# Optimization experiments

Measured on AMD Instinct MI355X. Metric: run time of the kernel, lower is better.

## Reference

```python
import jax, jax.numpy as jnp
import numpy as np

B, T, C, H = 256, 256, 384, 64
MAX_REL = 3  # max_relative_position hardcoded in module


def setup_inputs() -> dict:
    key = jax.random.key(0)
    ks = jax.random.split(key, 6)
    s = 1.0 / np.sqrt(C)
    return {
        "x": jax.random.normal(ks[0], (B, T, C), dtype=jnp.float32),
        "Wq": jax.random.normal(ks[1], (C, H), dtype=jnp.float32) * s,
        "Wk": jax.random.normal(ks[2], (C, H), dtype=jnp.float32) * s,
        "Wv": jax.random.normal(ks[3], (C, H), dtype=jnp.float32) * s,
        "rel_k_table": jax.random.normal(ks[4], (2 * MAX_REL + 1, H), dtype=jnp.float32) * s,
        "rel_v_table": jax.random.normal(ks[5], (2 * MAX_REL + 1, H), dtype=jnp.float32) * s,
    }


def reference(x, Wq, Wk, Wv, rel_k_table, rel_v_table):
    Bd, Td, Cd = x.shape
    Hd = Wq.shape[1]
    q = x @ Wq  # [B,T,H]
    k = x @ Wk
    v = x @ Wv
    # relative position indices, clipped Shaw-style
    r = jnp.arange(Td)
    idx = jnp.clip(r[None, :] - r[:, None], -MAX_REL, MAX_REL) + MAX_REL  # [T,T]
    rk = rel_k_table[idx]  # [T,T,H]
    rv = rel_v_table[idx]  # [T,T,H]
    attn1 = jnp.einsum('bth,bsh->bts', q, k)
    attn2 = jnp.einsum('bth,tsh->bts', q, rk)
    scale = jnp.sqrt(jnp.asarray(Hd, dtype=x.dtype))
    scores = (attn1 + attn2) / scale
    causal = jnp.tril(jnp.ones((Td, Td), dtype=bool))
    scores = jnp.where(causal[None, :, :], scores, -jnp.inf)
    attn = jax.nn.softmax(scores, axis=-1)  # dropout = identity (eval mode)
    w1 = jnp.einsum('bts,bsh->bth', attn, v)
    w2 = jnp.einsum('bts,tsh->bth', attn, rv)
    return w1 + w2  # [B,T,H]
```

## Files before the change

### kernel.cpp

```cpp
#include <hip/hip_runtime.h>
#include <hip/hip_bf16.h>


typedef __attribute__((ext_vector_type(8))) __bf16 bf16x8;
typedef __attribute__((ext_vector_type(8))) short short8;
typedef __attribute__((ext_vector_type(4))) float f32x4;
typedef __attribute__((ext_vector_type(4))) int   i32x4;

#define MFMA16(A, B, C) __builtin_amdgcn_mfma_f32_16x16x32_bf16((A), (B), (C), 0, 0, 0)

__device__ __forceinline__ unsigned short f2bf(float f) {
    unsigned int u = __builtin_bit_cast(unsigned int, f);
    u = (u + 0x7FFFu + ((u >> 16) & 1u)) >> 16;
    return (unsigned short)u;
}
__device__ __forceinline__ float bf2f(unsigned short s) {
    unsigned int u = ((unsigned int)s) << 16;
    return __builtin_bit_cast(float, u);
}
__device__ __forceinline__ bf16x8 ld16(const unsigned short* p) {
    return __builtin_bit_cast(bf16x8, *(const i32x4*)p);
}

__global__ void prep_wt(const float* __restrict__ Wq, const float* __restrict__ Wk,
                        const float* __restrict__ Wv, const float* __restrict__ relk,
                        unsigned short* __restrict__ Wt, unsigned short* __restrict__ Rk) {
    int i = blockIdx.x * 256 + threadIdx.x;
    if (i < 3 * 64 * 384) {
        int kk = i % 384;
        int h  = (i / 384) & 63;
        int w  = i / (384 * 64);
        const float* W = (w == 0) ? Wq : ((w == 1) ? Wk : Wv);
        Wt[i] = f2bf(W[kk * 64 + h]);
    } else if (i < 3 * 64 * 384 + 1024) {
        int j = i - 3 * 64 * 384;
        int n = j >> 6, h = j & 63;
        Rk[j] = (n < 4) ? f2bf(relk[n * 64 + h]) : (unsigned short)0;
    }
}

__global__ __launch_bounds__(512, 1) void qkv_kernel(
        const float* __restrict__ x, const unsigned short* __restrict__ Wt,
        unsigned short* __restrict__ q, unsigned short* __restrict__ k,
        unsigned short* __restrict__ vT) {
    extern __shared__ unsigned short ws[];

    const int tid  = threadIdx.x;
    const int wave = tid >> 6;
    const int lane = tid & 63;
    const int c    = lane & 15;
    const int quad = lane >> 4;
    const int row0 = blockIdx.x * 128;
    const int myrow = row0 + wave * 16 + c;

    const float* xp0 = x + (size_t)myrow * 384;

    f32x4 xb[2][8];
#pragma unroll
    for (int j = 0; j < 4; j++) {
        xb[0][2 * j]     = *(const f32x4*)(xp0 + j * 32 + quad * 8);
        xb[0][2 * j + 1] = *(const f32x4*)(xp0 + j * 32 + quad * 8 + 4);
    }

#pragma unroll
    for (int it = 0; it < 18; it++) {
        int P = it * 512 + tid;
        int r = P / 48, pc = P % 48;
        i32x4 d = *(const i32x4*)(Wt + r * 384 + pc * 8);
        *(i32x4*)(ws + r * 392 + pc * 8) = d;
    }
    __syncthreads();

    f32x4 zero = {0.f, 0.f, 0.f, 0.f};
    f32x4 aq[4], ak[4], av[4];
#pragma unroll
    for (int i = 0; i < 4; i++) { aq[i] = zero; ak[i] = zero; av[i] = zero; }

#pragma unroll
    for (int ck = 0; ck < 3; ck++) {
        const int cur = ck & 1;
        if (ck < 2) {
#pragma unroll
            for (int j = 0; j < 4; j++) {
                const float* xp = xp0 + (ck + 1) * 128 + j * 32 + quad * 8;
                xb[1 - cur][2 * j]     = *(const f32x4*)xp;
                xb[1 - cur][2 * j + 1] = *(const f32x4*)(xp + 4);
            }
        }
#pragma unroll
        for (int j = 0; j < 4; j++) {
            short8 xs8;
#pragma unroll
            for (int e = 0; e < 4; e++) {
                xs8[e]     = (short)f2bf(xb[cur][2 * j][e]);
                xs8[4 + e] = (short)f2bf(xb[cur][2 * j + 1][e]);
            }
            bf16x8 a = __builtin_bit_cast(bf16x8, xs8);
            const int col = (ck * 4 + j) * 32 + quad * 8;

#pragma unroll
            for (int nt = 0; nt < 4; nt++) {
                bf16x8 bq = ld16(ws + (nt * 16 + c) * 392 + col);
                bf16x8 bk = ld16(ws + (64 + nt * 16 + c) * 392 + col);
                bf16x8 aw = ld16(ws + (128 + nt * 16 + c) * 392 + col);
                aq[nt] = MFMA16(a, bq, aq[nt]);
                ak[nt] = MFMA16(a, bk, ak[nt]);
                av[nt] = MFMA16(aw, a, av[nt]);
            }
        }
    }

    const int b   = row0 >> 8;
    const int t0b = row0 & 255;
#pragma unroll
    for (int nt = 0; nt < 4; nt++) {
#pragma unroll
        for (int r = 0; r < 4; r++) {
            int row = row0 + wave * 16 + quad * 4 + r;
            q[row * 64 + nt * 16 + c] = f2bf(aq[nt][r]);
            k[row * 64 + nt * 16 + c] = f2bf(ak[nt][r]);
            int h = nt * 16 + quad * 4 + r;
            vT[(b * 64 + h) * 256 + t0b + wave * 16 + c] = f2bf(av[nt][r]);
        }
    }
}

__global__ __launch_bounds__(64, 4) void attn_kernel(
        const unsigned short* __restrict__ q, const unsigned short* __restrict__ k,
        const unsigned short* __restrict__ vT, const unsigned short* __restrict__ Rk,
        const float* __restrict__ relv, float* __restrict__ out) {
    __shared__ unsigned short P[16][264];
    __shared__ float E[16][4];

    const int lane = threadIdx.x;
    const int c    = lane & 15;
    const int quad = lane >> 4;
    const int tt   = blockIdx.x;
    const int b    = blockIdx.y;
    const int t0   = tt * 16;
    const int nst  = tt + 1;

    f32x4 zero = {0.f, 0.f, 0.f, 0.f};

    float rv[4][4];
#pragma unroll
    for (int j = 0; j < 4; j++)
#pragma unroll
        for (int nt = 0; nt < 4; nt++) rv[j][nt] = relv[j * 64 + nt * 16 + c];

    const unsigned short* qp = q + (size_t)(b * 256 + t0 + c) * 64 + quad * 8;
    bf16x8 aq0 = ld16(qp);
    bf16x8 aq1 = ld16(qp + 32);

    {
        f32x4 e = zero;
        e = MFMA16(aq0, ld16(Rk + c * 64 + quad * 8), e);
        e = MFMA16(aq1, ld16(Rk + c * 64 + 32 + quad * 8), e);
        if (c < 4) {
#pragma unroll
            for (int r = 0; r < 4; r++) E[quad * 4 + r][c] = e[r];
        }
    }
    __syncthreads();
    f32x4 ef[4];
#pragma unroll
    for (int r = 0; r < 4; r++) ef[r] = *(const f32x4*)(&E[quad * 4 + r][0]);

    float l[4] = {0.f, 0.f, 0.f, 0.f};
#pragma unroll
    for (int st = 0; st < 16; st++) {
        if (st < nst) {
            const unsigned short* kp = k + (size_t)(b * 256 + st * 16 + c) * 64 + quad * 8;
            f32x4 s = zero;
            s = MFMA16(aq0, ld16(kp), s);
            s = MFMA16(aq1, ld16(kp + 32), s);
#pragma unroll
            for (int r = 0; r < 4; r++) {
                int tg = t0 + quad * 4 + r;
                int sg = st * 16 + c;
                int d  = sg - tg;
                float e = (d <= -3) ? ef[r][0] : (d == -2) ? ef[r][1]
                        : (d == -1) ? ef[r][2] : ef[r][3];
                float p = (d > 0) ? 0.f : __expf(0.125f * (s[r] + e));
                l[r] += p;
                P[quad * 4 + r][sg] = f2bf(p);
            }
        }
    }
    if (nst & 1) {
#pragma unroll
        for (int r = 0; r < 4; r++) P[quad * 4 + r][nst * 16 + c] = 0;
    }
#pragma unroll
    for (int r = 0; r < 4; r++)
#pragma unroll
        for (int ofs = 1; ofs < 16; ofs <<= 1)
            l[r] += __shfl_xor(l[r], ofs, 64);
    float rl[4];
#pragma unroll
    for (int r = 0; r < 4; r++) rl[r] = 1.0f / l[r];
    __syncthreads();

    f32x4 o[4];
#pragma unroll
    for (int nt = 0; nt < 4; nt++) o[nt] = zero;
    const int ksteps = (nst + 1) >> 1;
#pragma unroll
    for (int ks = 0; ks < 8; ks++) {
        if (ks < ksteps) {
            bf16x8 ap = ld16(&P[c][ks * 32 + quad * 8]);
#pragma unroll
            for (int nt = 0; nt < 4; nt++) {
                const unsigned short* vp = vT + (size_t)(b * 64 + nt * 16 + c) * 256
                                              + ks * 32 + quad * 8;
                o[nt] = MFMA16(ap, ld16(vp), o[nt]);
            }
        }
    }

#pragma unroll
    for (int r = 0; r < 4; r++) {
        int tl = quad * 4 + r;
        int tg = t0 + tl;
        float pa = (tg >= 2) ? bf2f(P[tl][tg - 2]) * rl[r] : 0.f;
        float pb = (tg >= 1) ? bf2f(P[tl][tg - 1]) * rl[r] : 0.f;
        float pc = bf2f(P[tl][tg]) * rl[r];
#pragma unroll
        for (int nt = 0; nt < 4; nt++) {
            float r0 = rv[0][nt];
            float w2 = r0 + pa * (rv[1][nt] - r0) + pb * (rv[2][nt] - r0)
                          + pc * (rv[3][nt] - r0);
            out[(size_t)(b * 256 + tg) * 64 + nt * 16 + c] = o[nt][r] * rl[r] + w2;
        }
    }
}

extern "C" void kernel_launch(void* const* d_in, const int* in_sizes, int n_in,
                              void* d_out, int out_size, void* d_ws, size_t ws_size,
                              hipStream_t stream) {
    const float* x    = (const float*)d_in[0];
    const float* Wq   = (const float*)d_in[1];
    const float* Wk   = (const float*)d_in[2];
    const float* Wv   = (const float*)d_in[3];
    const float* relk = (const float*)d_in[4];
    const float* relv = (const float*)d_in[5];
    float* out = (float*)d_out;

    char* ws = (char*)d_ws;
    unsigned short* q  = (unsigned short*)(ws);
    unsigned short* kk = (unsigned short*)(ws + 8388608);
    unsigned short* vT = (unsigned short*)(ws + 16777216);
    unsigned short* Wt = (unsigned short*)(ws + 25165824);
    unsigned short* Rk = (unsigned short*)(ws + 25313280);

    (void)hipFuncSetAttribute((const void*)qkv_kernel,
                              hipFuncAttributeMaxDynamicSharedMemorySize, 150528);

    prep_wt<<<292, 256, 0, stream>>>(Wq, Wk, Wv, relk, Wt, Rk);
    qkv_kernel<<<512, 512, 150528, stream>>>(x, Wt, q, kk, vT);
    attn_kernel<<<dim3(16, 256), 64, 0, stream>>>(q, kk, vT, Rk, relv, out);
}
```

Before: 204.2 us.

## Fuse QKV projection and attention into one per-batch kernel with LDS-resident K/V

Merges the QKV projection and attention kernels into a single kernel with one 512-thread block per batch element. Q, K and V^T stay in shared memory instead of being written to and re-read from global memory. Each wave handles a pair of query tiles (w and 15-w) to balance the causal workload, and the weights are streamed into LDS in K-chunks. The cost is only 256 blocks with one block per CU and a large LDS footprint, so parallelism and latency hiding are reduced.

```diff
diff --git a/kernel.cpp b/kernel.cpp
--- a/kernel.cpp
+++ b/kernel.cpp
@@ -39,198 +39,209 @@
     }
 }
 
-__global__ __launch_bounds__(512, 1) void qkv_kernel(
+__global__ __launch_bounds__(512, 1) void fused_kernel(
         const float* __restrict__ x, const unsigned short* __restrict__ Wt,
-        unsigned short* __restrict__ q, unsigned short* __restrict__ k,
-        unsigned short* __restrict__ vT) {
-    extern __shared__ unsigned short ws[];
+        const unsigned short* __restrict__ Rk, const float* __restrict__ relv,
+        float* __restrict__ out) {
+    extern __shared__ unsigned short sh[];
+    unsigned short* ksh = sh;
+    unsigned short* vTs = sh + 18432;
+    unsigned short* qs  = sh + 35328;
+    unsigned short* wc  = sh + 53760;
 
     const int tid  = threadIdx.x;
     const int wave = tid >> 6;
     const int lane = tid & 63;
     const int c    = lane & 15;
     const int quad = lane >> 4;
-    const int row0 = blockIdx.x * 128;
-    const int myrow = row0 + wave * 16 + c;
-
-    const float* xp0 = x + (size_t)myrow * 384;
-
-    f32x4 xb[2][8];
-#pragma unroll
-    for (int j = 0; j < 4; j++) {
-        xb[0][2 * j]     = *(const f32x4*)(xp0 + j * 32 + quad * 8);
-        xb[0][2 * j + 1] = *(const f32x4*)(xp0 + j * 32 + quad * 8 + 4);
+    const int b    = blockIdx.x;
+
+    const f32x4 zero = {0.f, 0.f, 0.f, 0.f};
+
+    const float* xbase = x + (size_t)(b * 256 + wave * 32 + c) * 384 + quad * 8;
+
+    f32x4 aq[2][4], ak[2][4], av[2][4];
+#pragma unroll
+    for (int rt = 0; rt < 2; rt++)
+#pragma unroll
+        for (int nt = 0; nt < 4; nt++) { aq[rt][nt] = zero; ak[rt][nt] = zero; av[rt][nt] = zero; }
+
+    f32x4 tmp[2][8];
+#pragma unroll
+    for (int rt = 0; rt < 2; rt++)
+#pragma unroll
+        for (int j = 0; j < 4; j++) {
+            const float* xp = xbase + rt * 6144 + j * 32;
+            tmp[rt][2 * j]     = *(const f32x4*)xp;
+            tmp[rt][2 * j + 1] = *(const f32x4*)(xp + 4);
+        }
+
+#pragma unroll
+    for (int ck = 0; ck < 3; ck++) {
+        if (ck) __syncthreads();
+#pragma unroll
+        for (int it = 0; it < 6; it++) {
+            int P_ = it * 512 + tid;
+            int r = P_ >> 4, pc = P_ & 15;
+            i32x4 d = *(const i32x4*)(Wt + r * 384 + ck * 128 + pc * 8);
+            *(i32x4*)(wc + r * 136 + pc * 8) = d;
+        }
+        __syncthreads();
+
+        bf16x8 a[2][4];
+#pragma unroll
+        for (int rt = 0; rt < 2; rt++)
+#pragma unroll
+            for (int j = 0; j < 4; j++) {
+                short8 xs8;
+#pragma unroll
+                for (int e = 0; e < 4; e++) {
+                    xs8[e]     = (short)f2bf(tmp[rt][2 * j][e]);
+                    xs8[4 + e] = (short)f2bf(tmp[rt][2 * j + 1][e]);
+                }
+                a[rt][j] = __builtin_bit_cast(bf16x8, xs8);
+            }
+        if (ck < 2) {
+#pragma unroll
+            for (int rt = 0; rt < 2; rt++)
+#pragma unroll
+                for (int j = 0; j < 4; j++) {
+                    const float* xp = xbase + rt * 6144 + (ck + 1) * 128 + j * 32;
+                    tmp[rt][2 * j]     = *(const f32x4*)xp;
+                    tmp[rt][2 * j + 1] = *(const f32x4*)(xp + 4);
+                }
+        }
+
+#pragma unroll
+        for (int j = 0; j < 4; j++) {
+            const int col = j * 32 + quad * 8;
+#pragma unroll
+            for (int nt = 0; nt < 4; nt++) {
+                bf16x8 bq = ld16(wc + (nt * 16 + c) * 136 + col);
+                bf16x8 bk = ld16(wc + (64 + nt * 16 + c) * 136 + col);
+                bf16x8 aw = ld16(wc + (128 + nt * 16 + c) * 136 + col);
+                aq[0][nt] = MFMA16(a[0][j], bq, aq[0][nt]);
+                aq[1][nt] = MFMA16(a[1][j], bq, aq[1][nt]);
+                ak[0][nt] = MFMA16(a[0][j], bk, ak[0][nt]);
+                ak[1][nt] = MFMA16(a[1][j], bk, ak[1][nt]);
+                av[0][nt] = MFMA16(aw, a[0][j], av[0][nt]);
+                av[1][nt] = MFMA16(aw, a[1][j], av[1][nt]);
+            }
+        }
     }
 
 #pragma unroll
-    for (int it = 0; it < 18; it++) {
-        int P = it * 512 + tid;
-        int r = P / 48, pc = P % 48;
-        i32x4 d = *(const i32x4*)(Wt + r * 384 + pc * 8);
-        *(i32x4*)(ws + r * 392 + pc * 8) = d;
-    }
+    for (int rt = 0; rt < 2; rt++)
+#pragma unroll
+        for (int nt = 0; nt < 4; nt++)
+#pragma unroll
+            for (int r = 0; r < 4; r++) {
+                int row = wave * 32 + rt * 16 + quad * 4 + r;
+                qs[row * 72 + nt * 16 + c]  = f2bf(aq[rt][nt][r]);
+                ksh[row * 72 + nt * 16 + c] = f2bf(ak[rt][nt][r]);
+                vTs[(nt * 16 + quad * 4 + r) * 264 + wave * 32 + rt * 16 + c] = f2bf(av[rt][nt][r]);
+            }
     __syncthreads();
 
-    f32x4 zero = {0.f, 0.f, 0.f, 0.f};
-    f32x4 aq[4], ak[4], av[4];
-#pragma unroll
-    for (int i = 0; i < 4; i++) { aq[i] = zero; ak[i] = zero; av[i] = zero; }
-
-#pragma unroll
-    for (int ck = 0; ck < 3; ck++) {
-        const int cur = ck & 1;
-        if (ck < 2) {
-#pragma unroll
-            for (int j = 0; j < 4; j++) {
-                const float* xp = xp0 + (ck + 1) * 128 + j * 32 + quad * 8;
-                xb[1 - cur][2 * j]     = *(const f32x4*)xp;
-                xb[1 - cur][2 * j + 1] = *(const f32x4*)(xp + 4);
-            }
-        }
-#pragma unroll
-        for (int j = 0; j < 4; j++) {
-            short8 xs8;
-#pragma unroll
-            for (int e = 0; e < 4; e++) {
-                xs8[e]     = (short)f2bf(xb[cur][2 * j][e]);
-                xs8[4 + e] = (short)f2bf(xb[cur][2 * j + 1][e]);
-            }
-            bf16x8 a = __builtin_bit_cast(bf16x8, xs8);
-            const int col = (ck * 4 + j) * 32 + quad * 8;
-
-#pragma unroll
-            for (int nt = 0; nt < 4; nt++) {
-                bf16x8 bq = ld16(ws + (nt * 16 + c) * 392 + col);
-                bf16x8 bk = ld16(ws + (64 + nt * 16 + c) * 392 + col);
-                bf16x8 aw = ld16(ws + (128 + nt * 16 + c) * 392 + col);
-                aq[nt] = MFMA16(a, bq, aq[nt]);
-                ak[nt] = MFMA16(a, bk, ak[nt]);
-                av[nt] = MFMA16(aw, a, av[nt]);
-            }
-        }
-    }
-
-    const int b   = row0 >> 8;
-    const int t0b = row0 & 255;
-#pragma unroll
-    for (int nt = 0; nt < 4; nt++) {
-#pragma unroll
-        for (int r = 0; r < 4; r++) {
-            int row = row0 + wave * 16 + quad * 4 + r;
-            q[row * 64 + nt * 16 + c] = f2bf(aq[nt][r]);
-            k[row * 64 + nt * 16 + c] = f2bf(ak[nt][r]);
-            int h = nt * 16 + quad * 4 + r;
-            vT[(b * 64 + h) * 256 + t0b + wave * 16 + c] = f2bf(av[nt][r]);
-        }
-    }
-}
-
-__global__ __launch_bounds__(64, 4) void attn_kernel(
-        const unsigned short* __restrict__ q, const unsigned short* __restrict__ k,
-        const unsigned short* __restrict__ vT, const unsigned short* __restrict__ Rk,
-        const float* __restrict__ relv, float* __restrict__ out) {
-    __shared__ unsigned short P[16][264];
-    __shared__ float E[16][4];
-
-    const int lane = threadIdx.x;
-    const int c    = lane & 15;
-    const int quad = lane >> 4;
-    const int tt   = blockIdx.x;
-    const int b    = blockIdx.y;
-    const int t0   = tt * 16;
-    const int nst  = tt + 1;
-
-    f32x4 zero = {0.f, 0.f, 0.f, 0.f};
-
+    const int tA = wave, tB = 15 - wave;
+    bf16x8 qA0 = ld16(qs + (tA * 16 + c) * 72 + quad * 8);
+    bf16x8 qA1 = ld16(qs + (tA * 16 + c) * 72 + 32 + quad * 8);
+    bf16x8 qB0 = ld16(qs + (tB * 16 + c) * 72 + quad * 8);
+    bf16x8 qB1 = ld16(qs + (tB * 16 + c) * 72 + 32 + quad * 8);
     float rv[4][4];
 #pragma unroll
     for (int j = 0; j < 4; j++)
 #pragma unroll
         for (int nt = 0; nt < 4; nt++) rv[j][nt] = relv[j * 64 + nt * 16 + c];
-
-    const unsigned short* qp = q + (size_t)(b * 256 + t0 + c) * 64 + quad * 8;
-    bf16x8 aq0 = ld16(qp);
-    bf16x8 aq1 = ld16(qp + 32);
-
-    {
+    __syncthreads();
+
+    unsigned short* Pw = sh + 35328 + wave * 4224;
+
+#pragma unroll
+    for (int it2 = 0; it2 < 2; it2++) {
+        const int tt  = it2 ? tB : tA;
+        const bf16x8 aq0 = it2 ? qB0 : qA0;
+        const bf16x8 aq1 = it2 ? qB1 : qA1;
+        const int nst = tt + 1;
+
         f32x4 e = zero;
         e = MFMA16(aq0, ld16(Rk + c * 64 + quad * 8), e);
         e = MFMA16(aq1, ld16(Rk + c * 64 + 32 + quad * 8), e);
-        if (c < 4) {
-#pragma unroll
-            for (int r = 0; r < 4; r++) E[quad * 4 + r][c] = e[r];
-        }
-    }
-    __syncthreads();
-    f32x4 ef[4];
-#pragma unroll
-    for (int r = 0; r < 4; r++) ef[r] = *(const f32x4*)(&E[quad * 4 + r][0]);
-
-    float l[4] = {0.f, 0.f, 0.f, 0.f};
-#pragma unroll
-    for (int st = 0; st < 16; st++) {
-        if (st < nst) {
-            const unsigned short* kp = k + (size_t)(b * 256 + st * 16 + c) * 64 + quad * 8;
-            f32x4 s = zero;
-            s = MFMA16(aq0, ld16(kp), s);
-            s = MFMA16(aq1, ld16(kp + 32), s);
-#pragma unroll
-            for (int r = 0; r < 4; r++) {
-                int tg = t0 + quad * 4 + r;
-                int sg = st * 16 + c;
-                int d  = sg - tg;
-                float e = (d <= -3) ? ef[r][0] : (d == -2) ? ef[r][1]
-                        : (d == -1) ? ef[r][2] : ef[r][3];
-                float p = (d > 0) ? 0.f : __expf(0.125f * (s[r] + e));
-                l[r] += p;
-                P[quad * 4 + r][sg] = f2bf(p);
-            }
-        }
-    }
-    if (nst & 1) {
-#pragma unroll
-        for (int r = 0; r < 4; r++) P[quad * 4 + r][nst * 16 + c] = 0;
-    }
-#pragma unroll
-    for (int r = 0; r < 4; r++)
-#pragma unroll
-        for (int ofs = 1; ofs < 16; ofs <<= 1)
-            l[r] += __shfl_xor(l[r], ofs, 64);
-    float rl[4];
-#pragma unroll
-    for (int r = 0; r < 4; r++) rl[r] = 1.0f / l[r];
-    __syncthreads();
-
-    f32x4 o[4];
-#pragma unroll
-    for (int nt = 0; nt < 4; nt++) o[nt] = zero;
-    const int ksteps = (nst + 1) >> 1;
-#pragma unroll
-    for (int ks = 0; ks < 8; ks++) {
-        if (ks < ksteps) {
-            bf16x8 ap = ld16(&P[c][ks * 32 + quad * 8]);
+        float ef[4][4];
+#pragma unroll
+        for (int r = 0; r < 4; r++)
+#pragma unroll
+            for (int n = 0; n < 4; n++)
+                ef[r][n] = __shfl(e[r], (lane & 48) + n, 64);
+
+        __asm__ __volatile__("s_waitcnt lgkmcnt(0)" ::: "memory");
+
+        float l[4] = {0.f, 0.f, 0.f, 0.f};
+#pragma unroll
+        for (int st = 0; st < 16; st++) {
+            if (st < nst) {
+                const unsigned short* kp = ksh + (st * 16 + c) * 72 + quad * 8;
+                f32x4 s = zero;
+                s = MFMA16(aq0, ld16(kp), s);
+                s = MFMA16(aq1, ld16(kp + 32), s);
+#pragma unroll
+                for (int r = 0; r < 4; r++) {
+                    int tg = tt * 16 + quad * 4 + r;
+                    int sg = st * 16 + c;
+                    int d  = sg - tg;
+                    float ee = (d <= -3) ? ef[r][0] : (d == -2) ? ef[r][1]
+                             : (d == -1) ? ef[r][2] : ef[r][3];
+                    float p = (d > 0) ? 0.f : __expf(0.125f * (s[r] + ee));
+                    l[r] += p;
+                    Pw[(quad * 4 + r) * 264 + sg] = f2bf(p);
+                }
+            }
+        }
+        if (nst & 1) {
+#pragma unroll
+            for (int r = 0; r < 4; r++) Pw[(quad * 4 + r) * 264 + nst * 16 + c] = 0;
+        }
+#pragma unroll
+        for (int r = 0; r < 4; r++)
+#pragma unroll
+            for (int ofs = 1; ofs < 16; ofs <<= 1)
+                l[r] += __shfl_xor(l[r], ofs, 64);
+        float rl[4];
+#pragma unroll
+        for (int r = 0; r < 4; r++) rl[r] = 1.0f / l[r];
+
+        __asm__ __volatile__("s_waitcnt lgkmcnt(0)" ::: "memory");
+
+        f32x4 o[4];
+#pragma unroll
+        for (int nt = 0; nt < 4; nt++) o[nt] = zero;
+        const int ksteps = (nst + 1) >> 1;
+#pragma unroll
+        for (int ks = 0; ks < 8; ks++) {
+            if (ks < ksteps) {
+                bf16x8 ap = ld16(Pw + c * 264 + ks * 32 + quad * 8);
+#pragma unroll
+                for (int nt = 0; nt < 4; nt++) {
+                    bf16x8 bv = ld16(vTs + (nt * 16 + c) * 264 + ks * 32 + quad * 8);
+                    o[nt] = MFMA16(ap, bv, o[nt]);
+                }
+            }
+        }
+
+#pragma unroll
+        for (int r = 0; r < 4; r++) {
+            int tl = quad * 4 + r;
+            int tg = tt * 16 + tl;
+            float pa  = (tg >= 2) ? bf2f(Pw[tl * 264 + tg - 2]) * rl[r] : 0.f;
+            float pb  = (tg >= 1) ? bf2f(Pw[tl * 264 + tg - 1]) * rl[r] : 0.f;
+            float pcv = bf2f(Pw[tl * 264 + tg]) * rl[r];
 #pragma unroll
             for (int nt = 0; nt < 4; nt++) {
-                const unsigned short* vp = vT + (size_t)(b * 64 + nt * 16 + c) * 256
-                                              + ks * 32 + quad * 8;
-                o[nt] = MFMA16(ap, ld16(vp), o[nt]);
-            }
-        }
-    }
-
-#pragma unroll
-    for (int r = 0; r < 4; r++) {
-        int tl = quad * 4 + r;
-        int tg = t0 + tl;
-        float pa = (tg >= 2) ? bf2f(P[tl][tg - 2]) * rl[r] : 0.f;
-        float pb = (tg >= 1) ? bf2f(P[tl][tg - 1]) * rl[r] : 0.f;
-        float pc = bf2f(P[tl][tg]) * rl[r];
-#pragma unroll
-        for (int nt = 0; nt < 4; nt++) {
-            float r0 = rv[0][nt];
-            float w2 = r0 + pa * (rv[1][nt] - r0) + pb * (rv[2][nt] - r0)
-                          + pc * (rv[3][nt] - r0);
-            out[(size_t)(b * 256 + tg) * 64 + nt * 16 + c] = o[nt][r] * rl[r] + w2;
+                float r0 = rv[0][nt];
+                float w2 = r0 + pa * (rv[1][nt] - r0) + pb * (rv[2][nt] - r0)
+                              + pcv * (rv[3][nt] - r0);
+                out[(size_t)(b * 256 + tg) * 64 + nt * 16 + c] = o[nt][r] * rl[r] + w2;
+            }
         }
     }
 }
@@ -247,16 +258,12 @@
     float* out = (float*)d_out;
 
     char* ws = (char*)d_ws;
-    unsigned short* q  = (unsigned short*)(ws);
-    unsigned short* kk = (unsigned short*)(ws + 8388608);
-    unsigned short* vT = (unsigned short*)(ws + 16777216);
-    unsigned short* Wt = (unsigned short*)(ws + 25165824);
-    unsigned short* Rk = (unsigned short*)(ws + 25313280);
-
-    (void)hipFuncSetAttribute((const void*)qkv_kernel,
-                              hipFuncAttributeMaxDynamicSharedMemorySize, 150528);
+    unsigned short* Wt = (unsigned short*)(ws);
+    unsigned short* Rk = (unsigned short*)(ws + 147456);
+
+    (void)hipFuncSetAttribute((const void*)fused_kernel,
+                              hipFuncAttributeMaxDynamicSharedMemorySize, 159744);
 
     prep_wt<<<292, 256, 0, stream>>>(Wq, Wk, Wv, relk, Wt, Rk);
-    qkv_kernel<<<512, 512, 150528, stream>>>(x, Wt, q, kk, vT);
-    attn_kernel<<<dim3(16, 256), 64, 0, stream>>>(q, kk, vT, Rk, relv, out);
-}
+    fused_kernel<<<256, 512, 159744, stream>>>(x, Wt, Rk, relv, out);
+}
```

Result: faster. 197.0 us (-3.6%).
